# Performance work log

Hardware: AMD Instinct MI355X
Metric: run time of the kernel (lower is better)

Reference implementation:

```python
import jax, jax.numpy as jnp
import numpy as np

DIM = 512
HEADS = 8
HD = DIM // HEADS
WS = 4          # window_size
SHIFT = 2       # window_size // 2
HID = 4 * DIM   # mlp hidden
EPS = 1e-5


def _ln(x, g, b):
    m = jnp.mean(x, axis=-1, keepdims=True)
    v = jnp.mean((x - m) ** 2, axis=-1, keepdims=True)
    return (x - m) * jax.lax.rsqrt(v + EPS) * g + b


def setup_inputs() -> dict:
    key = jax.random.key(0)
    ks = jax.random.split(key, 12)
    s = 0.02
    return {
        "x": jax.random.normal(ks[0], (2, 32, 32, 32, DIM), dtype=jnp.float32),
        "ln1_g": jnp.ones((DIM,), jnp.float32),
        "ln1_b": jnp.zeros((DIM,), jnp.float32),
        "qkv_w": jax.random.normal(ks[1], (DIM, 3 * DIM), jnp.float32) * s,
        "qkv_b": jnp.zeros((3 * DIM,), jnp.float32),
        "proj_w": jax.random.normal(ks[2], (DIM, DIM), jnp.float32) * s,
        "proj_b": jnp.zeros((DIM,), jnp.float32),
        "ln2_g": jnp.ones((DIM,), jnp.float32),
        "ln2_b": jnp.zeros((DIM,), jnp.float32),
        "ffn_w1": jax.random.normal(ks[3], (DIM, HID), jnp.float32) * s,
        "ffn_b1": jnp.zeros((HID,), jnp.float32),
        "ffn_w2": jax.random.normal(ks[4], (HID, DIM), jnp.float32) * s,
        "ffn_b2": jnp.zeros((DIM,), jnp.float32),
    }


def reference(x, ln1_g, ln1_b, qkv_w, qkv_b, proj_w, proj_b,
              ln2_g, ln2_b, ffn_w1, ffn_b1, ffn_w2, ffn_b2):
    B, D, H, W, C = x.shape
    nD, nH, nW = D // WS, H // WS, W // WS
    N = WS ** 3

    # cyclic shift
    xs = jnp.roll(x, (-SHIFT, -SHIFT, -SHIFT), axis=(1, 2, 3))

    # window partition: (B*numWin, N, C)
    xw = xs.reshape(B, nD, WS, nH, WS, nW, WS, C)
    xw = xw.transpose(0, 1, 3, 5, 2, 4, 6, 7).reshape(-1, N, C)

    # pre-norm attention
    h = _ln(xw, ln1_g, ln1_b)
    qkv = (h @ qkv_w + qkv_b).reshape(-1, N, 3, HEADS, HD)
    q, k, v = jnp.moveaxis(qkv, 2, 0)          # each (Bn, N, HEADS, HD)
    scale = HD ** -0.5
    logits = jnp.einsum('bnhd,bmhd->bhnm', q, k) * scale
    attn = jax.nn.softmax(logits, axis=-1)
    out = jnp.einsum('bhnm,bmhd->bnhd', attn, v).reshape(-1, N, C)
    out = out @ proj_w + proj_b
    xw = xw + out

    # window reverse + unshift
    xo = xw.reshape(B, nD, nH, nW, WS, WS, WS, C)
    xo = xo.transpose(0, 1, 4, 2, 5, 3, 6, 7).reshape(B, D, H, W, C)
    xo = jnp.roll(xo, (SHIFT, SHIFT, SHIFT), axis=(1, 2, 3))

    # pre-norm FFN (exact GELU, dropout inactive in eval)
    h2 = _ln(xo, ln2_g, ln2_b)
    ffn = jax.nn.gelu(h2 @ ffn_w1 + ffn_b1, approximate=False) @ ffn_w2 + ffn_b2
    return xo + ffn
```

## Files before the change

### kernel.cpp

```cpp
#include <hip/hip_runtime.h>
#include <hip/hip_bf16.h>


typedef __attribute__((ext_vector_type(4))) short short4v;
typedef __attribute__((ext_vector_type(8))) short short8v;
typedef __attribute__((ext_vector_type(4))) float f32x4;

__device__ __forceinline__ unsigned short f2bf(float f) {
  unsigned u = __float_as_uint(f);
  u += 0x7fffu + ((u >> 16) & 1u);
  return (unsigned short)(u >> 16);
}

__device__ __forceinline__ void gload_lds16(const unsigned short* g, unsigned short* l) {
  __builtin_amdgcn_global_load_lds(
      (const __attribute__((address_space(1))) unsigned int*)g,
      (__attribute__((address_space(3))) unsigned int*)l, 16, 0, 0);
}

__global__ __launch_bounds__(256)
void wprep_all(const float* __restrict__ qkv_w, const float* __restrict__ proj_w,
               const float* __restrict__ w1, const float* __restrict__ w2,
               unsigned short* __restrict__ wt) {
  int idx = blockIdx.x * 256 + threadIdx.x;
  const float* w; int kbits, N, base;
  if (idx < 786432)       { w = qkv_w;  kbits = 9;  N = 1536; base = 0; }
  else if (idx < 1048576) { w = proj_w; kbits = 9;  N = 512;  base = 786432; }
  else if (idx < 2097152) { w = w1;     kbits = 9;  N = 2048; base = 1048576; }
  else                    { w = w2;     kbits = 11; N = 512;  base = 2097152; }
  int li = idx - base;
  int K = 1 << kbits;
  int n = li >> kbits, kk = li & (K - 1);
  wt[idx] = f2bf(w[(long)kk * N + n]);
}

__global__ __launch_bounds__(256)
void ln_kernel(const float* __restrict__ src, const float* __restrict__ g,
               const float* __restrict__ bb, unsigned short* __restrict__ dst,
               const int gather) {
  const int lane = threadIdx.x & 63;
  const int row = blockIdx.x * 4 + (threadIdx.x >> 6);
  long srow;
  if (gather) {
    int n = row & 63, win = row >> 6;
    int w0 = win & 7, h0 = (win >> 3) & 7, d0 = (win >> 6) & 7, b2 = win >> 9;
    int dx = n & 3, dy = (n >> 2) & 3, dz = n >> 4;
    int od = (d0 * 4 + dz + 2) & 31, oh = (h0 * 4 + dy + 2) & 31, ow = (w0 * 4 + dx + 2) & 31;
    srow = (((long)b2 * 32 + od) * 32 + oh) * 32 + ow;
  } else {
    srow = row;
  }
  const float4* sp = (const float4*)(src + srow * 512);
  float4 x0 = sp[lane], x1 = sp[lane + 64];
  float sum = x0.x + x0.y + x0.z + x0.w + x1.x + x1.y + x1.z + x1.w;
  float sq  = x0.x*x0.x + x0.y*x0.y + x0.z*x0.z + x0.w*x0.w
            + x1.x*x1.x + x1.y*x1.y + x1.z*x1.z + x1.w*x1.w;
#pragma unroll
  for (int off = 1; off < 64; off <<= 1) {
    sum += __shfl_xor(sum, off, 64);
    sq  += __shfl_xor(sq, off, 64);
  }
  float mean = sum * (1.0f / 512.0f);
  float var  = sq * (1.0f / 512.0f) - mean * mean;
  float rstd = rsqrtf(var + 1e-5f);
  float4 g0 = ((const float4*)g)[lane], g1 = ((const float4*)g)[lane + 64];
  float4 b0 = ((const float4*)bb)[lane], b1v = ((const float4*)bb)[lane + 64];
  ushort4 o0, o1;
  o0.x = f2bf((x0.x - mean) * rstd * g0.x + b0.x);
  o0.y = f2bf((x0.y - mean) * rstd * g0.y + b0.y);
  o0.z = f2bf((x0.z - mean) * rstd * g0.z + b0.z);
  o0.w = f2bf((x0.w - mean) * rstd * g0.w + b0.w);
  o1.x = f2bf((x1.x - mean) * rstd * g1.x + b1v.x);
  o1.y = f2bf((x1.y - mean) * rstd * g1.y + b1v.y);
  o1.z = f2bf((x1.z - mean) * rstd * g1.z + b1v.z);
  o1.w = f2bf((x1.w - mean) * rstd * g1.w + b1v.w);
  *(ushort4*)(dst + (long)row * 512 + lane * 4) = o0;
  *(ushort4*)(dst + (long)row * 512 + 256 + lane * 4) = o1;
}

template <int EPI>
__global__ __launch_bounds__(256)
void gemm_bt(const unsigned short* __restrict__ A,
             const unsigned short* __restrict__ Bt,
             const float* __restrict__ bias, int K,
             void* __restrict__ out0,
             unsigned short* __restrict__ out1,
             unsigned short* __restrict__ out2,
             const float* __restrict__ res) {
  __shared__ unsigned short As0[128 * 32], Bs0[128 * 32];
  __shared__ unsigned short As1[128 * 32], Bs1[128 * 32];
  const int tid = threadIdx.x;
  const int lane = tid & 63;
  const int wv = tid >> 6;
  const int quad = lane >> 4;
  const int l15 = lane & 15;
  const int wm = (wv >> 1) << 6;
  const int wn = (wv & 1) << 6;
  const long row0 = (long)blockIdx.y * 128;
  const long col0 = (long)blockIdx.x * 128;

  f32x4 acc[4][4] = {};

  const int srw = lane >> 2;
  const int sch = lane & 3;
  const int r0 = wv * 16 + srw, r1 = 64 + wv * 16 + srw;
  const unsigned short* gA0 = A  + (row0 + r0) * K + (sch ^ ((r0 >> 1) & 3)) * 8;
  const unsigned short* gA1 = A  + (row0 + r1) * K + (sch ^ ((r1 >> 1) & 3)) * 8;
  const unsigned short* gB0 = Bt + (col0 + r0) * K + (sch ^ ((r0 >> 1) & 3)) * 8;
  const unsigned short* gB1 = Bt + (col0 + r1) * K + (sch ^ ((r1 >> 1) & 3)) * 8;
  const int ld0 = (wv * 16) * 32, ld1 = (64 + wv * 16) * 32;

  int offA[4], offB[4];
#pragma unroll
  for (int t = 0; t < 4; ++t) {
    const int ra = wm + t * 16 + l15;
    offA[t] = ra * 32 + (quad ^ ((ra >> 1) & 3)) * 8;
    const int rb = wn + t * 16 + l15;
    offB[t] = rb * 32 + (quad ^ ((rb >> 1) & 3)) * 8;
  }

#define STAGE(AS, BS, kkx) do {                    \
    gload_lds16(gA0 + (kkx), &AS[ld0]);            \
    gload_lds16(gB0 + (kkx), &BS[ld0]);            \
    gload_lds16(gA1 + (kkx), &AS[ld1]);            \
    gload_lds16(gB1 + (kkx), &BS[ld1]);            \
  } while (0)

#define COMPUTE(AS, BS) do {                                                   \
    short8v af[4], bf[4];                                                      \
    _Pragma("unroll")                                                          \
    for (int t = 0; t < 4; ++t) {                                              \
      af[t] = *(const short8v*)&AS[offA[t]];                                   \
      bf[t] = *(const short8v*)&BS[offB[t]];                                   \
    }                                                                          \
    _Pragma("unroll")                                                          \
    for (int mt = 0; mt < 4; ++mt)                                             \
      _Pragma("unroll")                                                        \
      for (int nt = 0; nt < 4; ++nt)                                           \
        acc[mt][nt] = __builtin_amdgcn_mfma_f32_16x16x32_bf16(                 \
            af[mt], bf[nt], acc[mt][nt], 0, 0, 0);                             \
  } while (0)

  STAGE(As0, Bs0, 0);
  for (int kk = 0; kk < K; kk += 64) {
    __syncthreads();
    STAGE(As1, Bs1, kk + 32);
    COMPUTE(As0, Bs0);
    __syncthreads();
    if (kk + 64 < K) STAGE(As0, Bs0, kk + 64);
    COMPUTE(As1, Bs1);
  }
#undef STAGE
#undef COMPUTE

#pragma unroll
  for (int mt = 0; mt < 4; ++mt) {
#pragma unroll
    for (int nt = 0; nt < 4; ++nt) {
#pragma unroll
      for (int r = 0; r < 4; ++r) {
        const long gr = row0 + wm + mt * 16 + quad * 4 + r;
        const long gc = col0 + wn + nt * 16 + l15;
        float val = acc[mt][nt][r] + bias[gc];
        if (EPI == 0) {
          int which = (int)(gc >> 9), rem = (int)gc & 511;
          int head = rem >> 6, hd = rem & 63;
          long win = gr >> 6, n = gr & 63;
          long base = (win * 8 + head) * 4096;
          unsigned short bv = f2bf(val);
          if (which == 0)      ((unsigned short*)out0)[base + n * 64 + hd] = bv;
          else if (which == 1) out1[base + n * 64 + hd] = bv;
          else                 out2[base + hd * 64 + n] = bv;
        } else if (EPI == 1) {
          int win = (int)(gr >> 6), n = (int)gr & 63;
          int w0 = win & 7, h0 = (win >> 3) & 7, d0 = (win >> 6) & 7, b2 = win >> 9;
          int dx = n & 3, dy = (n >> 2) & 3, dz = n >> 4;
          int od = (d0 * 4 + dz + 2) & 31, oh = (h0 * 4 + dy + 2) & 31, ow = (w0 * 4 + dx + 2) & 31;
          long addr = ((((long)b2 * 32 + od) * 32 + oh) * 32 + ow) * 512 + gc;
          ((float*)out0)[addr] = res[addr] + val;
        } else if (EPI == 2) {
          float ge = 0.5f * val * (1.0f + erff(val * 0.70710678118654752f));
          ((unsigned short*)out0)[gr * 2048 + gc] = f2bf(ge);
        } else {
          long addr = gr * 512 + gc;
          ((float*)out0)[addr] = res[addr] + val;
        }
      }
    }
  }
}

__global__ __launch_bounds__(256)
void attn_kernel(const unsigned short* __restrict__ q,
                 const unsigned short* __restrict__ k,
                 const unsigned short* __restrict__ vt,
                 unsigned short* __restrict__ out) {
  __shared__ unsigned short Ps[4][64 * 72];
  const int lane = threadIdx.x & 63;
  const int wave = threadIdx.x >> 6;
  const int quad = lane >> 4;
  const int l15 = lane & 15;
  const int unit = blockIdx.x * 4 + wave;
  const int win = unit >> 3;
  const int head = unit & 7;
  const long base = (long)unit * 4096;

  f32x4 s[4][4] = {};
#pragma unroll
  for (int kk = 0; kk < 64; kk += 32) {
    short8v a[4], b[4];
#pragma unroll
    for (int t = 0; t < 4; ++t) {
      a[t] = *(const short8v*)(q + base + (t * 16 + l15) * 64 + kk + quad * 8);
      b[t] = *(const short8v*)(k + base + (t * 16 + l15) * 64 + kk + quad * 8);
    }
#pragma unroll
    for (int mt = 0; mt < 4; ++mt)
#pragma unroll
      for (int nt = 0; nt < 4; ++nt)
        s[mt][nt] = __builtin_amdgcn_mfma_f32_16x16x32_bf16(a[mt], b[nt], s[mt][nt], 0, 0, 0);
  }

  float lrow[4][4];
#pragma unroll
  for (int mt = 0; mt < 4; ++mt) {
#pragma unroll
    for (int r = 0; r < 4; ++r) {
      float v0 = s[mt][0][r] * 0.125f, v1 = s[mt][1][r] * 0.125f;
      float v2 = s[mt][2][r] * 0.125f, v3 = s[mt][3][r] * 0.125f;
      float mx = fmaxf(fmaxf(v0, v1), fmaxf(v2, v3));
#pragma unroll
      for (int off = 1; off < 16; off <<= 1) mx = fmaxf(mx, __shfl_xor(mx, off, 64));
      v0 = __expf(v0 - mx); v1 = __expf(v1 - mx);
      v2 = __expf(v2 - mx); v3 = __expf(v3 - mx);
      float sm = v0 + v1 + v2 + v3;
#pragma unroll
      for (int off = 1; off < 16; off <<= 1) sm += __shfl_xor(sm, off, 64);
      lrow[mt][r] = sm;
      int row = mt * 16 + quad * 4 + r;
      Ps[wave][row * 72 + 0 + l15]  = f2bf(v0);
      Ps[wave][row * 72 + 16 + l15] = f2bf(v1);
      Ps[wave][row * 72 + 32 + l15] = f2bf(v2);
      Ps[wave][row * 72 + 48 + l15] = f2bf(v3);
    }
  }
  __syncthreads();

  f32x4 o[4][4] = {};
#pragma unroll
  for (int kk = 0; kk < 64; kk += 32) {
    short8v a[4], b[4];
#pragma unroll
    for (int t = 0; t < 4; ++t) {
      a[t] = *(const short8v*)(&Ps[wave][(t * 16 + l15) * 72 + kk + quad * 8]);
      b[t] = *(const short8v*)(vt + base + (t * 16 + l15) * 64 + kk + quad * 8);
    }
#pragma unroll
    for (int mt = 0; mt < 4; ++mt)
#pragma unroll
      for (int nt = 0; nt < 4; ++nt)
        o[mt][nt] = __builtin_amdgcn_mfma_f32_16x16x32_bf16(a[mt], b[nt], o[mt][nt], 0, 0, 0);
  }

#pragma unroll
  for (int mt = 0; mt < 4; ++mt)
#pragma unroll
    for (int nt = 0; nt < 4; ++nt)
#pragma unroll
      for (int r = 0; r < 4; ++r) {
        int row = mt * 16 + quad * 4 + r;
        int col = nt * 16 + l15;
        float val = o[mt][nt][r] / lrow[mt][r];
        out[((long)win * 64 + row) * 512 + head * 64 + col] = f2bf(val);
      }
}

extern "C" void kernel_launch(void* const* d_in, const int* in_sizes, int n_in,
                              void* d_out, int out_size, void* d_ws, size_t ws_size,
                              hipStream_t stream) {
  const float* x      = (const float*)d_in[0];
  const float* ln1_g  = (const float*)d_in[1];
  const float* ln1_b  = (const float*)d_in[2];
  const float* qkv_w  = (const float*)d_in[3];
  const float* qkv_b  = (const float*)d_in[4];
  const float* proj_w = (const float*)d_in[5];
  const float* proj_b = (const float*)d_in[6];
  const float* ln2_g  = (const float*)d_in[7];
  const float* ln2_b  = (const float*)d_in[8];
  const float* w1     = (const float*)d_in[9];
  const float* b1     = (const float*)d_in[10];
  const float* w2     = (const float*)d_in[11];
  const float* b2     = (const float*)d_in[12];

  char* ws = (char*)d_ws;
  unsigned short* wt_all  = (unsigned short*)ws;
  unsigned short* wt_qkv  = (unsigned short*)(ws + 0);
  unsigned short* wt_proj = (unsigned short*)(ws + 1572864);
  unsigned short* wt_1    = (unsigned short*)(ws + 2097152);
  unsigned short* wt_2    = (unsigned short*)(ws + 4194304);
  float*          xo      = (float*)(ws + 8388608);
  unsigned short* h       = (unsigned short*)(ws + 142606336);
  unsigned short* attno   = (unsigned short*)(ws + 209715200);
  unsigned short* qb      = (unsigned short*)(ws + 276824064);
  unsigned short* kb      = (unsigned short*)(ws + 343932928);
  unsigned short* vb      = (unsigned short*)(ws + 411041792);
  unsigned short* hid     = (unsigned short*)(ws + 209715200);
  float* out = (float*)d_out;

  wprep_all<<<12288, 256, 0, stream>>>(qkv_w, proj_w, w1, w2, wt_all);

  ln_kernel<<<16384, 256, 0, stream>>>(x, ln1_g, ln1_b, h, 1);
  gemm_bt<0><<<dim3(12, 512), 256, 0, stream>>>(h, wt_qkv, qkv_b, 512, qb, kb, vb, nullptr);
  attn_kernel<<<2048, 256, 0, stream>>>(qb, kb, vb, attno);
  gemm_bt<1><<<dim3(4, 512), 256, 0, stream>>>(attno, wt_proj, proj_b, 512, xo, nullptr, nullptr, x);
  ln_kernel<<<16384, 256, 0, stream>>>(xo, ln2_g, ln2_b, h, 0);
  gemm_bt<2><<<dim3(16, 512), 256, 0, stream>>>(h, wt_1, b1, 512, hid, nullptr, nullptr, nullptr);
  gemm_bt<3><<<dim3(4, 512), 256, 0, stream>>>(hid, wt_2, b2, 2048, out, nullptr, nullptr, xo);
}
```

Baseline: 1.169 ms.

## Rewrite GEMM with 256x256 tiles, 8 waves, BK=64 and XCD-aware block remap

Replaces the 128x128, 4-wave, BK=32 GEMM with a 256x256 tile computed by 8 waves, each owning a 128x64 sub-tile. It uses a BK=64 double-buffered LDS pipeline with XOR swizzle and interleaves staging of the next A and B tiles between MFMA phases, using barriers and s_setprio. Blocks are remapped so that consecutive tiles land on the same XCD for L2 reuse. This raises arithmetic intensity and reduces global traffic, at the cost of 128KB of LDS per block, more registers, and fewer blocks for tail balancing.

```diff
diff --git a/kernel.cpp b/kernel.cpp
--- a/kernel.cpp
+++ b/kernel.cpp
@@ -79,7 +79,7 @@
 }
 
 template <int EPI>
-__global__ __launch_bounds__(256)
+__global__ __launch_bounds__(512, 2)
 void gemm_bt(const unsigned short* __restrict__ A,
              const unsigned short* __restrict__ Bt,
              const float* __restrict__ bias, int K,
@@ -87,80 +87,134 @@
              unsigned short* __restrict__ out1,
              unsigned short* __restrict__ out2,
              const float* __restrict__ res) {
-  __shared__ unsigned short As0[128 * 32], Bs0[128 * 32];
-  __shared__ unsigned short As1[128 * 32], Bs1[128 * 32];
+  __shared__ unsigned short As[2][256 * 64];
+  __shared__ unsigned short Bs[2][256 * 64];
   const int tid = threadIdx.x;
   const int lane = tid & 63;
   const int wv = tid >> 6;
+  const int wm = wv >> 2;
+  const int wn = wv & 3;
   const int quad = lane >> 4;
   const int l15 = lane & 15;
-  const int wm = (wv >> 1) << 6;
-  const int wn = (wv & 1) << 6;
-  const long row0 = (long)blockIdx.y * 128;
-  const long col0 = (long)blockIdx.x * 128;
-
-  f32x4 acc[4][4] = {};
-
-  const int srw = lane >> 2;
-  const int sch = lane & 3;
-  const int r0 = wv * 16 + srw, r1 = 64 + wv * 16 + srw;
-  const unsigned short* gA0 = A  + (row0 + r0) * K + (sch ^ ((r0 >> 1) & 3)) * 8;
-  const unsigned short* gA1 = A  + (row0 + r1) * K + (sch ^ ((r1 >> 1) & 3)) * 8;
-  const unsigned short* gB0 = Bt + (col0 + r0) * K + (sch ^ ((r0 >> 1) & 3)) * 8;
-  const unsigned short* gB1 = Bt + (col0 + r1) * K + (sch ^ ((r1 >> 1) & 3)) * 8;
-  const int ld0 = (wv * 16) * 32, ld1 = (64 + wv * 16) * 32;
-
-  int offA[4], offB[4];
-#pragma unroll
-  for (int t = 0; t < 4; ++t) {
-    const int ra = wm + t * 16 + l15;
-    offA[t] = ra * 32 + (quad ^ ((ra >> 1) & 3)) * 8;
-    const int rb = wn + t * 16 + l15;
-    offB[t] = rb * 32 + (quad ^ ((rb >> 1) & 3)) * 8;
-  }
-
-#define STAGE(AS, BS, kkx) do {                    \
-    gload_lds16(gA0 + (kkx), &AS[ld0]);            \
-    gload_lds16(gB0 + (kkx), &BS[ld0]);            \
-    gload_lds16(gA1 + (kkx), &AS[ld1]);            \
-    gload_lds16(gB1 + (kkx), &BS[ld1]);            \
+
+  const int gx = gridDim.x;
+  const int nwg = gx * gridDim.y;
+  const int bid = blockIdx.y * gx + blockIdx.x;
+  const int cpx = nwg >> 3;
+  const int wg2 = (bid & 7) * cpx + (bid >> 3);
+  const int bx = wg2 % gx;
+  const int by = wg2 / gx;
+  const long row0 = (long)by * 256;
+  const long col0 = (long)bx * 256;
+
+  f32x4 acc[8][4] = {};
+
+  const int srow = wv * 8 + (lane >> 3);
+  const int scg  = (lane & 7) ^ (lane >> 3);
+  const unsigned short* gA = A  + (row0 + srow) * K + scg * 8;
+  const unsigned short* gB = Bt + (col0 + srow) * K + scg * 8;
+  const long jmp = 64L * K;
+  const int ldst = wv * 512;
+
+#define STAGE_A(buf, koff) do {                                         \
+    _Pragma("unroll")                                                   \
+    for (int j = 0; j < 4; ++j)                                         \
+      gload_lds16(gA + (koff) + j * jmp, &As[buf][ldst + j * 4096]);    \
   } while (0)
-
-#define COMPUTE(AS, BS) do {                                                   \
-    short8v af[4], bf[4];                                                      \
-    _Pragma("unroll")                                                          \
-    for (int t = 0; t < 4; ++t) {                                              \
-      af[t] = *(const short8v*)&AS[offA[t]];                                   \
-      bf[t] = *(const short8v*)&BS[offB[t]];                                   \
-    }                                                                          \
-    _Pragma("unroll")                                                          \
-    for (int mt = 0; mt < 4; ++mt)                                             \
-      _Pragma("unroll")                                                        \
-      for (int nt = 0; nt < 4; ++nt)                                           \
-        acc[mt][nt] = __builtin_amdgcn_mfma_f32_16x16x32_bf16(                 \
-            af[mt], bf[nt], acc[mt][nt], 0, 0, 0);                             \
+#define STAGE_B(buf, koff) do {                                         \
+    _Pragma("unroll")                                                   \
+    for (int j = 0; j < 4; ++j)                                         \
+      gload_lds16(gB + (koff) + j * jmp, &Bs[buf][ldst + j * 4096]);    \
   } while (0)
 
-  STAGE(As0, Bs0, 0);
-  for (int kk = 0; kk < K; kk += 64) {
-    __syncthreads();
-    STAGE(As1, Bs1, kk + 32);
-    COMPUTE(As0, Bs0);
-    __syncthreads();
-    if (kk + 64 < K) STAGE(As0, Bs0, kk + 64);
-    COMPUTE(As1, Bs1);
-  }
-#undef STAGE
-#undef COMPUTE
-
-#pragma unroll
-  for (int mt = 0; mt < 4; ++mt) {
+  const int co0 = ((quad)     ^ (l15 & 7)) * 8;
+  const int co1 = ((quad + 4) ^ (l15 & 7)) * 8;
+  const int aB0 = (wm * 128 + l15) * 64 + co0;
+  const int aB1 = (wm * 128 + l15) * 64 + co1;
+  const int bB0 = (wn * 64 + l15) * 64 + co0;
+  const int bB1 = (wn * 64 + l15) * 64 + co1;
+
+#define MFMA_ROW(mh)                                                    \
+    _Pragma("unroll")                                                   \
+    for (int i = 0; i < 4; ++i)                                         \
+      _Pragma("unroll")                                                 \
+      for (int nt = 0; nt < 4; ++nt)                                    \
+        acc[(mh) * 4 + i][nt] = __builtin_amdgcn_mfma_f32_16x16x32_bf16( \
+            af[i], bfrag[nt], acc[(mh) * 4 + i][nt], 0, 0, 0)
+
+  const int nk = K >> 6;
+  STAGE_A(0, 0);
+  STAGE_B(0, 0);
+  asm volatile("s_waitcnt vmcnt(0)" ::: "memory");
+  __builtin_amdgcn_s_barrier();
+
+  for (int t = 0; t < nk; ++t) {
+    const int cur = t & 1, nxt = cur ^ 1;
+    const int more = (t + 1 < nk);
+    const int kn = (t + 1) << 6;
+    const unsigned short* Ac = As[cur];
+    const unsigned short* Bc = Bs[cur];
+    short8v bfrag[4];
+    {
+      short8v af[4];
+#pragma unroll
+      for (int nt = 0; nt < 4; ++nt) bfrag[nt] = *(const short8v*)&Bc[bB0 + nt * 1024];
+#pragma unroll
+      for (int i = 0; i < 4; ++i) af[i] = *(const short8v*)&Ac[aB0 + i * 1024];
+      if (more) STAGE_A(nxt, kn);
+      __builtin_amdgcn_s_barrier();
+      __builtin_amdgcn_s_setprio(1);
+      MFMA_ROW(0);
+      __builtin_amdgcn_s_setprio(0);
+      __builtin_amdgcn_s_barrier();
+    }
+    {
+      short8v af[4];
+#pragma unroll
+      for (int i = 0; i < 4; ++i) af[i] = *(const short8v*)&Ac[aB0 + (4 + i) * 1024];
+      if (more) STAGE_B(nxt, kn);
+      __builtin_amdgcn_s_barrier();
+      __builtin_amdgcn_s_setprio(1);
+      MFMA_ROW(1);
+      __builtin_amdgcn_s_setprio(0);
+      __builtin_amdgcn_s_barrier();
+    }
+    {
+      short8v af[4];
+#pragma unroll
+      for (int nt = 0; nt < 4; ++nt) bfrag[nt] = *(const short8v*)&Bc[bB1 + nt * 1024];
+#pragma unroll
+      for (int i = 0; i < 4; ++i) af[i] = *(const short8v*)&Ac[aB1 + i * 1024];
+      __builtin_amdgcn_s_barrier();
+      __builtin_amdgcn_s_setprio(1);
+      MFMA_ROW(0);
+      __builtin_amdgcn_s_setprio(0);
+      __builtin_amdgcn_s_barrier();
+    }
+    {
+      short8v af[4];
+#pragma unroll
+      for (int i = 0; i < 4; ++i) af[i] = *(const short8v*)&Ac[aB1 + (4 + i) * 1024];
+      __builtin_amdgcn_s_barrier();
+      __builtin_amdgcn_s_setprio(1);
+      MFMA_ROW(1);
+      __builtin_amdgcn_s_setprio(0);
+      asm volatile("s_waitcnt vmcnt(0)" ::: "memory");
+      __builtin_amdgcn_s_barrier();
+    }
+  }
+#undef STAGE_A
+#undef STAGE_B
+#undef MFMA_ROW
+
+#pragma unroll
+  for (int mt = 0; mt < 8; ++mt) {
 #pragma unroll
     for (int nt = 0; nt < 4; ++nt) {
 #pragma unroll
       for (int r = 0; r < 4; ++r) {
-        const long gr = row0 + wm + mt * 16 + quad * 4 + r;
-        const long gc = col0 + wn + nt * 16 + l15;
+        const long gr = row0 + wm * 128 + mt * 16 + quad * 4 + r;
+        const long gc = col0 + wn * 64 + nt * 16 + l15;
         float val = acc[mt][nt][r] + bias[gc];
         if (EPI == 0) {
           int which = (int)(gc >> 9), rem = (int)gc & 511;
@@ -310,10 +364,10 @@
   wprep_all<<<12288, 256, 0, stream>>>(qkv_w, proj_w, w1, w2, wt_all);
 
   ln_kernel<<<16384, 256, 0, stream>>>(x, ln1_g, ln1_b, h, 1);
-  gemm_bt<0><<<dim3(12, 512), 256, 0, stream>>>(h, wt_qkv, qkv_b, 512, qb, kb, vb, nullptr);
+  gemm_bt<0><<<dim3(6, 256), 512, 0, stream>>>(h, wt_qkv, qkv_b, 512, qb, kb, vb, nullptr);
   attn_kernel<<<2048, 256, 0, stream>>>(qb, kb, vb, attno);
-  gemm_bt<1><<<dim3(4, 512), 256, 0, stream>>>(attno, wt_proj, proj_b, 512, xo, nullptr, nullptr, x);
+  gemm_bt<1><<<dim3(2, 256), 512, 0, stream>>>(attno, wt_proj, proj_b, 512, xo, nullptr, nullptr, x);
   ln_kernel<<<16384, 256, 0, stream>>>(xo, ln2_g, ln2_b, h, 0);
-  gemm_bt<2><<<dim3(16, 512), 256, 0, stream>>>(h, wt_1, b1, 512, hid, nullptr, nullptr, nullptr);
-  gemm_bt<3><<<dim3(4, 512), 256, 0, stream>>>(hid, wt_2, b2, 2048, out, nullptr, nullptr, xo);
-}
+  gemm_bt<2><<<dim3(8, 256), 512, 0, stream>>>(h, wt_1, b1, 512, hid, nullptr, nullptr, nullptr);
+  gemm_bt<3><<<dim3(2, 256), 512, 0, stream>>>(hid, wt_2, b2, 2048, out, nullptr, nullptr, xo);
+}
```

Result: faster. 1.107 ms (-5.3%).
